# Kernel optimization log

Hardware: AMD Instinct MI355X
Metric: run time of the kernel (lower is better)

The kernel has to match this reference:

```python
import jax, jax.numpy as jnp
import numpy as np
import math

EPS = 1e-5
N_HEAD = 16

def act_quant(x):
    # BitNet per-token int8 absmax quant-dequant with straight-through estimator
    scale = 127.0 / jnp.clip(jnp.max(jnp.abs(x), axis=-1, keepdims=True), EPS)
    q = jnp.clip(jnp.round(x * scale), -128.0, 127.0) / scale
    return x + jax.lax.stop_gradient(q - x)

def bit_linear(x, W):
    # BitNet b1.58 ternary weight quant (per-tensor mean-absmax scale), STE
    s = jnp.clip(jnp.mean(jnp.abs(W)), EPS)
    Wq = jnp.clip(jnp.round(W / s), -1.0, 1.0) * s
    Wq = W + jax.lax.stop_gradient(Wq - W)
    return x @ Wq.T

def setup_inputs() -> dict:
    key = jax.random.key(0)
    ks = jax.random.split(key, 5)
    B, T, C = 2, 2048, 2048
    x = jax.random.normal(ks[0], (B, T, C), dtype=jnp.float32)
    std = 1.0 / math.sqrt(C)
    Wq = jax.random.normal(ks[1], (C, C), dtype=jnp.float32) * std
    Wk = jax.random.normal(ks[2], (C, C), dtype=jnp.float32) * std
    Wv = jax.random.normal(ks[3], (C, C), dtype=jnp.float32) * std
    Wp = jax.random.normal(ks[4], (C, C), dtype=jnp.float32) * std
    return {"x": x, "Wq": Wq, "Wk": Wk, "Wv": Wv, "Wp": Wp}

def reference(x, Wq, Wk, Wv, Wp):
    B, T, C = x.shape
    H = N_HEAD
    D = C // H
    xq = act_quant(x)
    # [B, T, C] -> [B, H, T, D]
    def heads(t):
        return t.reshape(B, T, H, D).transpose(0, 2, 1, 3)
    q = act_quant(heads(bit_linear(xq, Wq)))
    k = act_quant(heads(bit_linear(xq, Wk)))
    v = act_quant(heads(bit_linear(xq, Wv)))
    scores = jnp.einsum('bhtd,bhsd->bhts', q, k) * (1.0 / math.sqrt(D))
    w = act_quant(jax.nn.softmax(scores, axis=-1))  # dropout p=0.0 (eval)
    y = act_quant(jnp.einsum('bhts,bhsd->bhtd', w, v))
    y = y.transpose(0, 2, 1, 3).reshape(B, T, C)
    y = act_quant(bit_linear(y, Wp))
    return y
```

## Files before the change

kernel.cpp:

```cpp
#include <hip/hip_runtime.h>
#include <stdint.h>

namespace {

constexpr int B_ = 2, T_ = 2048, C_ = 2048, H_ = 16, D_ = 128;
constexpr int R_ = B_ * T_;
constexpr float EPSF = 1e-5f;
constexpr float INV_SQRT_D = 0.08838834764831845f;
constexpr float LOG2E = 1.4426950408889634f;
constexpr float LOG2_127 = 6.988684686772166f;

constexpr size_t OFF_WSUM = 0;
constexpr size_t OFF_SW   = 64;
constexpr size_t OFF_WT   = 256;
constexpr size_t OFF_XQ   = OFF_WT   + (size_t)4 * C_ * C_;
constexpr size_t OFF_SX   = OFF_XQ   + (size_t)R_ * C_;
constexpr size_t OFF_QKV  = OFF_SX   + (size_t)R_ * 4;
constexpr size_t OFF_SQKV = OFF_QKV  + (size_t)3 * R_ * C_;
constexpr size_t OFF_YQ   = OFF_SQKV + (size_t)3 * R_ * H_ * 4;
constexpr size_t OFF_SY   = OFF_YQ   + (size_t)R_ * C_;
constexpr size_t OFF_OUTP = OFF_SY   + (size_t)R_ * H_ * 4;
constexpr size_t OFF_VT   = OFF_OUTP;

typedef int   i32x4 __attribute__((ext_vector_type(4)));
typedef short s16x8 __attribute__((ext_vector_type(8)));
typedef float f32x4 __attribute__((ext_vector_type(4)));
typedef unsigned int u32x4 __attribute__((ext_vector_type(4)));

__device__ __forceinline__ i32x4 mfma_i8(i32x4 a, i32x4 b, i32x4 c) {
  return __builtin_amdgcn_mfma_i32_16x16x64_i8(a, b, c, 0, 0, 0);
}
__device__ __forceinline__ f32x4 mfma_bf16(s16x8 a, s16x8 b, f32x4 c) {
  return __builtin_amdgcn_mfma_f32_16x16x32_bf16(a, b, c, 0, 0, 0);
}

__device__ __forceinline__ void dma16(const void* g, void* l) {
  __builtin_amdgcn_global_load_lds(
      (const __attribute__((address_space(1))) void*)g,
      (__attribute__((address_space(3))) void*)l, 16, 0, 0);
}

#if __has_builtin(__builtin_amdgcn_exp2f)
__device__ __forceinline__ float fast_exp2(float x) { return __builtin_amdgcn_exp2f(x); }
#else
__device__ __forceinline__ float fast_exp2(float x) { return exp2f(x); }
#endif

__device__ __forceinline__ short f2bf(float f) {
  union { float f; uint32_t u; } v; v.f = f;
  uint32_t r = v.u + 0x7fffu + ((v.u >> 16) & 1u);
  return (short)(r >> 16);
}
__device__ __forceinline__ float bf2f(short h) {
  union { uint32_t u; float f; } v; v.u = ((uint32_t)(uint16_t)h) << 16;
  return v.f;
}

__global__ __launch_bounds__(256) void wabs_sum_kernel(
    const float* __restrict__ W0, const float* __restrict__ W1,
    const float* __restrict__ W2, const float* __restrict__ W3,
    double* __restrict__ wsum)
{
  const int w   = blockIdx.x >> 6;
  const int blk = blockIdx.x & 63;
  const float* W = (w == 0) ? W0 : (w == 1) ? W1 : (w == 2) ? W2 : W3;
  const float4* W4 = (const float4*)W;
  const int n4 = (C_ * C_) / 4;
  double s = 0.0;
  for (int i = blk * 256 + (int)threadIdx.x; i < n4; i += 64 * 256) {
    float4 v = W4[i];
    s += (double)fabsf(v.x) + (double)fabsf(v.y) +
         (double)fabsf(v.z) + (double)fabsf(v.w);
  }
  __shared__ double sm[256];
  sm[threadIdx.x] = s;
  __syncthreads();
  for (int o = 128; o > 0; o >>= 1) {
    if ((int)threadIdx.x < o) sm[threadIdx.x] += sm[threadIdx.x + o];
    __syncthreads();
  }
  if (threadIdx.x == 0) atomicAdd(&wsum[w], sm[0]);
}

__global__ __launch_bounds__(256) void wquant_kernel(
    const float* __restrict__ W0, const float* __restrict__ W1,
    const float* __restrict__ W2, const float* __restrict__ W3,
    const double* __restrict__ wsum, int8_t* __restrict__ Wt, float* __restrict__ sw)
{
  const int w = blockIdx.x >> 10;
  const float* W = (w == 0) ? W0 : (w == 1) ? W1 : (w == 2) ? W2 : W3;
  const int n = C_ * C_;
  const int n4 = n / 4;
  const float s = fmaxf((float)(wsum[w] * (1.0 / (double)n)), EPSF);
  const float4* W4 = (const float4*)W;
  uint32_t* dst4 = (uint32_t*)(Wt + (size_t)w * n);
  const int base = (blockIdx.x & 1023) * 256 + (int)threadIdx.x;
  for (int i = base; i < n4; i += 1024 * 256) {
    float4 v = W4[i];
    union { int8_t b[4]; uint32_t u; } pk;
    pk.b[0] = (int8_t)fminf(fmaxf(rintf(v.x / s), -1.f), 1.f);
    pk.b[1] = (int8_t)fminf(fmaxf(rintf(v.y / s), -1.f), 1.f);
    pk.b[2] = (int8_t)fminf(fmaxf(rintf(v.z / s), -1.f), 1.f);
    pk.b[3] = (int8_t)fminf(fmaxf(rintf(v.w / s), -1.f), 1.f);
    dst4[i] = pk.u;
  }
  if (base == 0) sw[w] = s;
}

__global__ __launch_bounds__(256) void xquant_kernel(
    const float* __restrict__ x, int8_t* __restrict__ xq, float* __restrict__ sx)
{
  const int r = blockIdx.x;
  const float4* xr = (const float4*)(x + (size_t)r * C_);
  float am = 0.f;
  for (int j = threadIdx.x; j < C_ / 4; j += 256) {
    float4 v = xr[j];
    am = fmaxf(am, fmaxf(fmaxf(fabsf(v.x), fabsf(v.y)),
                         fmaxf(fabsf(v.z), fabsf(v.w))));
  }
  __shared__ float sm[256];
  sm[threadIdx.x] = am;
  __syncthreads();
  for (int o = 128; o > 0; o >>= 1) {
    if ((int)threadIdx.x < o) sm[threadIdx.x] = fmaxf(sm[threadIdx.x], sm[threadIdx.x + o]);
    __syncthreads();
  }
  const float m = fmaxf(sm[0], EPSF);
  const float scale = 127.f / m;
  uint32_t* dst4 = (uint32_t*)(xq + (size_t)r * C_);
  for (int j = threadIdx.x; j < C_ / 4; j += 256) {
    float4 v = xr[j];
    union { int8_t b[4]; uint32_t u; } pk;
    pk.b[0] = (int8_t)fminf(fmaxf(rintf(v.x * scale), -128.f), 127.f);
    pk.b[1] = (int8_t)fminf(fmaxf(rintf(v.y * scale), -128.f), 127.f);
    pk.b[2] = (int8_t)fminf(fmaxf(rintf(v.z * scale), -128.f), 127.f);
    pk.b[3] = (int8_t)fminf(fmaxf(rintf(v.w * scale), -128.f), 127.f);
    dst4[j] = pk.u;
  }
  if (threadIdx.x == 0) sx[r] = m / 127.f;
}

__global__ __launch_bounds__(256) void proj_mfma_kernel(
    const int8_t* __restrict__ xq, const float* __restrict__ sx,
    const int8_t* __restrict__ Wt, const float* __restrict__ sw4,
    int8_t* __restrict__ qkv, float* __restrict__ sqkv)
{
  const int h    = blockIdx.x;
  const int r0   = blockIdx.y * 128;
  const int wsel = blockIdx.z;
  const int tid  = (int)threadIdx.x;
  const int wv   = tid >> 6;
  const int lane = tid & 63;
  const int quad = lane >> 4;
  const int l15  = lane & 15;
  const int rh   = wv >> 1, ch = wv & 1;
  const int8_t* Wm = Wt + (size_t)wsel * C_ * C_;

  __shared__ __align__(16) char As[2][8192];
  __shared__ __align__(16) char Bs[2][8192];
  __shared__ int rmaxs[128];
  if (tid < 128) rmaxs[tid] = 0;

  const int s0a   = wv * 128;
  const int rowA0 = (s0a + lane) >> 2;
  const int qdA0  = ((s0a + lane) & 3) ^ (rowA0 & 3);
  const int rowA1 = (s0a + 64 + lane) >> 2;
  const int qdA1  = ((s0a + 64 + lane) & 3) ^ (rowA1 & 3);

  auto stage = [&](int bf, int k0) {
    dma16(xq + (size_t)(r0 + rowA0) * C_ + k0 + qdA0 * 16, &As[bf][(s0a) * 16]);
    dma16(xq + (size_t)(r0 + rowA1) * C_ + k0 + qdA1 * 16, &As[bf][(s0a + 64) * 16]);
    dma16(Wm + (size_t)(h * 128 + rowA0) * C_ + k0 + qdA0 * 16, &Bs[bf][(s0a) * 16]);
    dma16(Wm + (size_t)(h * 128 + rowA1) * C_ + k0 + qdA1 * 16, &Bs[bf][(s0a + 64) * 16]);
  };

  i32x4 acc[4][4];
  #pragma unroll
  for (int i = 0; i < 4; ++i)
    #pragma unroll
    for (int j = 0; j < 4; ++j) acc[i][j] = i32x4{0, 0, 0, 0};

  stage(0, 0);
  for (int kc = 0; kc < 32; ++kc) {
    __syncthreads();
    if (kc + 1 < 32) stage((kc + 1) & 1, (kc + 1) * 64);
    const char* Ab = As[kc & 1];
    const char* Bb = Bs[kc & 1];
    i32x4 a[4], b[4];
    #pragma unroll
    for (int rt = 0; rt < 4; ++rt) {
      const int row = rh * 64 + rt * 16 + l15;
      a[rt] = *(const i32x4*)(Ab + (row * 4 + (quad ^ (row & 3))) * 16);
    }
    #pragma unroll
    for (int ct = 0; ct < 4; ++ct) {
      const int col = ch * 64 + ct * 16 + l15;
      b[ct] = *(const i32x4*)(Bb + (col * 4 + (quad ^ (col & 3))) * 16);
    }
    #pragma unroll
    for (int rt = 0; rt < 4; ++rt)
      #pragma unroll
      for (int ct = 0; ct < 4; ++ct)
        acc[rt][ct] = mfma_i8(a[rt], b[ct], acc[rt][ct]);
  }

  #pragma unroll
  for (int rt = 0; rt < 4; ++rt)
    #pragma unroll
    for (int r = 0; r < 4; ++r) {
      int m = 0;
      #pragma unroll
      for (int ct = 0; ct < 4; ++ct) {
        int v = acc[rt][ct][r];
        int av = v < 0 ? -v : v;
        m = m > av ? m : av;
      }
      #pragma unroll
      for (int mm = 1; mm < 16; mm <<= 1) {
        int o = __shfl_xor(m, mm, 64);
        m = m > o ? m : o;
      }
      if (l15 == 0) atomicMax(&rmaxs[rh * 64 + rt * 16 + quad * 4 + r], m);
    }
  __syncthreads();

  const float swv = sw4[wsel];
  #pragma unroll
  for (int rt = 0; rt < 4; ++rt)
    #pragma unroll
    for (int r = 0; r < 4; ++r) {
      const int rowl = rh * 64 + rt * 16 + quad * 4 + r;
      const int rglob = r0 + rowl;
      const int mN = rmaxs[rowl];
      const float qscale = (mN > 0) ? 127.f / (float)mN : 0.f;
      const int bb = rglob >> 11;
      const int tt = rglob & (T_ - 1);
      const size_t obase = ((size_t)(bb * H_ + h) * T_ + tt) * D_;
      #pragma unroll
      for (int ct = 0; ct < 4; ++ct) {
        const int col = ch * 64 + ct * 16 + l15;
        float q = rintf((float)acc[rt][ct][r] * qscale);
        q = fminf(fmaxf(q, -128.f), 127.f);
        qkv[(size_t)wsel * R_ * C_ + obase + col] = (int8_t)q;
      }
      if (ch == 0 && l15 == 0) {
        float maxq = (float)mN * sx[rglob] * swv;
        sqkv[(size_t)wsel * R_ * H_ + (size_t)(bb * H_ + h) * T_ + tt] =
            fmaxf(maxq, EPSF) / 127.f;
      }
    }
}

__global__ __launch_bounds__(256) void vtrans_kernel(
    const int8_t* __restrict__ vq, const float* __restrict__ sv,
    short* __restrict__ vT)
{
  const int bh = blockIdx.y;
  const int s0 = blockIdx.x * 64;
  const int tid = (int)threadIdx.x;
  __shared__ __align__(16) int8_t Vs[64][144];
  __shared__ float svs[64];
  const int8_t* vbase = vq + ((size_t)bh * T_ + s0) * D_;
  #pragma unroll
  for (int it = 0; it < 2; ++it) {
    int idx = tid + it * 256;
    int row = idx >> 3, seg = idx & 7;
    *(uint4*)(&Vs[row][seg * 16]) = *(const uint4*)(vbase + row * 128 + seg * 16);
  }
  if (tid < 64) svs[tid] = sv[(size_t)bh * T_ + s0 + tid];
  __syncthreads();
  const int d    = tid >> 1;
  const int half = tid & 1;
  const int kh   = half * 32;
  uint32_t oh[16], ol[16];
  #pragma unroll
  for (int i = 0; i < 32; i += 2) {
    const int k0 = kh + i, k1 = kh + i + 1;
    float v0 = (float)(int)Vs[k0][d] * svs[k0];
    float v1 = (float)(int)Vs[k1][d] * svs[k1];
    short h0 = f2bf(v0), h1 = f2bf(v1);
    short l0 = f2bf(v0 - bf2f(h0)), l1 = f2bf(v1 - bf2f(h1));
    oh[i >> 1] = (uint32_t)(uint16_t)h0 | ((uint32_t)(uint16_t)h1 << 16);
    ol[i >> 1] = (uint32_t)(uint16_t)l0 | ((uint32_t)(uint16_t)l1 << 16);
  }
  const int c = (s0 >> 5) + half;
  char* out = (char*)vT + ((((size_t)bh * 128 + d) * 64 + (size_t)c) << 7);
  const int par = d & 7;
  #pragma unroll
  for (int g = 0; g < 4; ++g) {
    uint4 hi, lo;
    hi.x = oh[2 * g];     hi.y = oh[2 * g + 1];
    hi.z = oh[2 * g + 8]; hi.w = oh[2 * g + 9];
    lo.x = ol[2 * g];     lo.y = ol[2 * g + 1];
    lo.z = ol[2 * g + 8]; lo.w = ol[2 * g + 9];
    *(uint4*)(out + (((2 * g + par) & 7) << 4))     = hi;
    *(uint4*)(out + (((2 * g + 1 + par) & 7) << 4)) = lo;
  }
}

__global__ __launch_bounds__(256, 2) void attn_mfma_kernel(
    const int8_t* __restrict__ qq, const int8_t* __restrict__ kq,
    const float* __restrict__ sq, const float* __restrict__ sk,
    const short* __restrict__ vT,
    int8_t* __restrict__ yq, float* __restrict__ sy)
{
  const int bh  = blockIdx.x;
  const int t0  = blockIdx.y * 128;
  const int tid = (int)threadIdx.x;
  const int w    = tid >> 6;
  const int lane = tid & 63;
  const int quad = lane >> 4;
  const int l15  = lane & 15;

  __shared__ __align__(16) char smem[69632];
  float* sks = (float*)(smem + 61440);

  const int qrow0 = t0 + 32 * w;

  const int8_t* kq_bh = kq + (size_t)bh * T_ * D_;
  const char*   vb    = (const char*)vT + ((size_t)bh << 20);

  const int kslot = w * 64 + lane;
  const int kkey  = kslot >> 3;
  const int ksrc  = ((kslot & 7) ^ (kkey & 7)) * 16;
  auto stageK = [&](int buf, int cc) {
    dma16(kq_bh + (size_t)(cc * 32 + kkey) * 128 + ksrc,
          smem + buf * 4096 + (w * 64) * 16);
  };

  const size_t vlane = (size_t)(w * 32 + (lane >> 3)) * 8192 + (size_t)((lane & 7) * 16);
  auto stageV = [&](int buf, int cc) {
    char* dst = smem + 12288 + buf * 16384 + (w * 32) * 128;
    const char* src = vb + vlane + (size_t)cc * 128;
    #pragma unroll
    for (int j = 0; j < 4; ++j)
      dma16(src + (size_t)(j * 8) * 8192, dst + j * 1024);
  };

  {
    const float* skg = sk + (size_t)bh * T_;
    dma16(skg + (w * 2 + 0) * 256 + lane * 4, smem + 61440 + (w * 2 + 0) * 1024);
    dma16(skg + (w * 2 + 1) * 256 + lane * 4, smem + 61440 + (w * 2 + 1) * 1024);
  }
  stageK(0, 0);
  stageV(0, 0);

  i32x4 qf[2][2];
  #pragma unroll
  for (int qt = 0; qt < 2; ++qt)
    #pragma unroll
    for (int hf = 0; hf < 2; ++hf)
      qf[qt][hf] = *(const i32x4*)(qq + ((size_t)bh * T_ + qrow0 + qt * 16 + l15) * D_ +
                                   hf * 64 + quad * 16);
  float f0[2];
  #pragma unroll
  for (int qt = 0; qt < 2; ++qt)
    f0[qt] = sq[(size_t)bh * T_ + qrow0 + qt * 16 + l15] * INV_SQRT_D;

  __syncthreads();

  const int8_t* kqb = kq_bh + (size_t)(l15 * D_ + quad * 16);

  float rx[2][4];
  #pragma unroll
  for (int qt = 0; qt < 2; ++qt)
    #pragma unroll
    for (int r = 0; r < 4; ++r) rx[qt][r] = -3e38f;

  for (int s0 = 0; s0 < T_; s0 += 64) {
    #pragma unroll
    for (int kt = 0; kt < 4; ++kt) {
      const f32x4 skv = *(const f32x4*)(sks + s0 + kt * 16 + quad * 4);
      const i32x4 ka = *(const i32x4*)(kqb + (size_t)(s0 + kt * 16) * D_);
      const i32x4 kb = *(const i32x4*)(kqb + (size_t)(s0 + kt * 16) * D_ + 64);
      #pragma unroll
      for (int qt = 0; qt < 2; ++qt) {
        i32x4 c = i32x4{0, 0, 0, 0};
        c = mfma_i8(ka, qf[qt][0], c);
        c = mfma_i8(kb, qf[qt][1], c);
        #pragma unroll
        for (int r = 0; r < 4; ++r)
          rx[qt][r] = fmaxf(rx[qt][r], (float)c[r] * skv[r]);
      }
    }
  }
  float f1[2], g[2];
  #pragma unroll
  for (int qt = 0; qt < 2; ++qt) {
    float m = fmaxf(fmaxf(rx[qt][0], rx[qt][1]), fmaxf(rx[qt][2], rx[qt][3]));
    m = fmaxf(m, __shfl_xor(m, 16, 64));
    m = fmaxf(m, __shfl_xor(m, 32, 64));
    f1[qt] = f0[qt] * LOG2E;
    g[qt]  = LOG2_127 - (m * f0[qt]) * LOG2E;
  }

  float zac[2][4] = {};
  f32x4 yacc[2][8];
  #pragma unroll
  for (int qt = 0; qt < 2; ++qt)
    #pragma unroll
    for (int dt = 0; dt < 8; ++dt) yacc[qt][dt] = f32x4{0.f, 0.f, 0.f, 0.f};

  const int seg_hi = ((2 * quad + l15) & 7) << 4;
  const int seg_lo = ((2 * quad + 1 + l15) & 7) << 4;

  int bc = 0, bn = 1;
  for (int c = 0; c < 64; ++c) {
    const int s0k = c * 32;
    if (c + 1 < 64) {
      stageK(bn, c + 1);
      stageV(bn, c + 1);
      asm volatile("s_waitcnt vmcnt(5)" ::: "memory");
    } else {
      asm volatile("s_waitcnt vmcnt(0)" ::: "memory");
    }
    __builtin_amdgcn_s_barrier();
    asm volatile("" ::: "memory");

    const char* Kb = smem + bc * 4096;
    uint32_t wdw[2][2][2];
    #pragma unroll
    for (int kt = 0; kt < 2; ++kt) {
      const f32x4 skv = *(const f32x4*)(sks + s0k + kt * 16 + quad * 4);
      const int key = kt * 16 + l15;
      const i32x4 ka = *(const i32x4*)(Kb + key * 128 + ((quad ^ (key & 7)) << 4));
      const i32x4 kb = *(const i32x4*)(Kb + key * 128 + (((quad + 4) ^ (key & 7)) << 4));
      #pragma unroll
      for (int qt = 0; qt < 2; ++qt) {
        i32x4 cc = i32x4{0, 0, 0, 0};
        cc = mfma_i8(ka, qf[qt][0], cc);
        cc = mfma_i8(kb, qf[qt][1], cc);
        float wq_[4];
        #pragma unroll
        for (int r = 0; r < 4; ++r) {
          float t = (float)cc[r] * skv[r];
          float wu = fast_exp2(fmaf(t, f1[qt], g[qt]));
          zac[qt][r] += wu;
          wq_[r] = rintf(wu);
        }
        wdw[qt][kt][0] = (__float_as_uint(wq_[0]) >> 16) |
                         (__float_as_uint(wq_[1]) & 0xffff0000u);
        wdw[qt][kt][1] = (__float_as_uint(wq_[2]) >> 16) |
                         (__float_as_uint(wq_[3]) & 0xffff0000u);
      }
    }

    s16x8 wf[2];
    #pragma unroll
    for (int qt = 0; qt < 2; ++qt) {
      u32x4 tw;
      tw[0] = wdw[qt][0][0]; tw[1] = wdw[qt][0][1];
      tw[2] = wdw[qt][1][0]; tw[3] = wdw[qt][1][1];
      wf[qt] = __builtin_bit_cast(s16x8, tw);
    }

    const char* Vc = smem + 12288 + bc * 16384;
    __builtin_amdgcn_s_setprio(1);
    #pragma unroll
    for (int dt = 0; dt < 8; ++dt) {
      const char* rowp = Vc + (dt * 16 + l15) * 128;
      const s16x8 vh = *(const s16x8*)(rowp + seg_hi);
      const s16x8 vl = *(const s16x8*)(rowp + seg_lo);
      yacc[0][dt] = mfma_bf16(wf[0], vh, yacc[0][dt]);
      yacc[0][dt] = mfma_bf16(wf[0], vl, yacc[0][dt]);
      yacc[1][dt] = mfma_bf16(wf[1], vh, yacc[1][dt]);
      yacc[1][dt] = mfma_bf16(wf[1], vl, yacc[1][dt]);
    }
    __builtin_amdgcn_s_setprio(0);

    bc = bn; bn = (bn == 2) ? 0 : bn + 1;
  }

  float zq[2];
  #pragma unroll
  for (int qt = 0; qt < 2; ++qt) {
    float z = (zac[qt][0] + zac[qt][1]) + (zac[qt][2] + zac[qt][3]);
    z += __shfl_xor(z, 16, 64);
    z += __shfl_xor(z, 32, 64);
    zq[qt] = z;
  }

  const int b = bh >> 4;
  const int h = bh & 15;
  #pragma unroll
  for (int qt = 0; qt < 2; ++qt)
    #pragma unroll
    for (int r = 0; r < 4; ++r) {
      const float zr = __shfl(zq[qt], quad * 4 + r, 64);
      float ym = 0.f;
      #pragma unroll
      for (int dt = 0; dt < 8; ++dt) ym = fmaxf(ym, fabsf(yacc[qt][dt][r]));
      #pragma unroll
      for (int mm = 1; mm < 16; mm <<= 1) ym = fmaxf(ym, __shfl_xor(ym, mm, 64));
      const float invz = 1.f / zr;
      const float ymt = fmaxf(ym * invz, EPSF);
      const float fs = 127.f / ymt;
      const int tglob = t0 + 32 * w + qt * 16 + quad * 4 + r;
      const size_t rowbase = ((size_t)(b * T_ + tglob)) * C_ + h * D_;
      #pragma unroll
      for (int dt = 0; dt < 8; ++dt) {
        float yv = yacc[qt][dt][r] * invz;
        float qv = fminf(fmaxf(rintf(yv * fs), -128.f), 127.f);
        yq[rowbase + dt * 16 + l15] = (int8_t)qv;
      }
      if (l15 == 0)
        sy[(size_t)(b * T_ + tglob) * H_ + h] = ymt / 127.f;
    }
}

__global__ __launch_bounds__(256) void outproj_mfma_kernel(
    const int8_t* __restrict__ yq, const float* __restrict__ sy,
    const int8_t* __restrict__ Wt, const float* __restrict__ sw4,
    float* __restrict__ outp)
{
  const int n0  = blockIdx.x * 64;
  const int r0  = blockIdx.y * 128;
  const int tid = (int)threadIdx.x;
  const int wv   = tid >> 6;
  const int lane = tid & 63;
  const int quad = lane >> 4;
  const int l15  = lane & 15;
  const int rh   = wv >> 1, ch = wv & 1;
  const int8_t* Wm = Wt + (size_t)3 * C_ * C_;

  __shared__ __align__(16) char As[2][8192];
  __shared__ __align__(16) char Bs[2][4096];
  __shared__ float sYs[128][16];
  for (int idx = tid; idx < 128 * 16; idx += 256)
    sYs[idx >> 4][idx & 15] = sy[(size_t)(r0 + (idx >> 4)) * H_ + (idx & 15)];

  const int s0a   = wv * 128;
  const int rowA0 = (s0a + lane) >> 2;
  const int qdA0  = ((s0a + lane) & 3) ^ (rowA0 & 3);
  const int rowA1 = (s0a + 64 + lane) >> 2;
  const int qdA1  = ((s0a + 64 + lane) & 3) ^ (rowA1 & 3);
  const int sb    = wv * 64 + lane;
  const int colB  = sb >> 2;
  const int qdB   = (sb & 3) ^ (colB & 3);

  auto stage = [&](int bf, int k0) {
    dma16(yq + (size_t)(r0 + rowA0) * C_ + k0 + qdA0 * 16, &As[bf][(s0a) * 16]);
    dma16(yq + (size_t)(r0 + rowA1) * C_ + k0 + qdA1 * 16, &As[bf][(s0a + 64) * 16]);
    dma16(Wm + (size_t)(n0 + colB) * C_ + k0 + qdB * 16, &Bs[bf][(wv * 64) * 16]);
  };

  i32x4 iacc[4][2];
  f32x4 facc[4][2];
  #pragma unroll
  for (int i = 0; i < 4; ++i)
    #pragma unroll
    for (int j = 0; j < 2; ++j) { iacc[i][j] = i32x4{0,0,0,0}; facc[i][j] = f32x4{0.f,0.f,0.f,0.f}; }

  stage(0, 0);
  for (int kc = 0; kc < 32; ++kc) {
    __syncthreads();
    if (kc + 1 < 32) stage((kc + 1) & 1, (kc + 1) * 64);
    const char* Ab = As[kc & 1];
    const char* Bb = Bs[kc & 1];
    i32x4 a[4], b[2];
    #pragma unroll
    for (int rt = 0; rt < 4; ++rt) {
      const int row = rh * 64 + rt * 16 + l15;
      a[rt] = *(const i32x4*)(Ab + (row * 4 + (quad ^ (row & 3))) * 16);
    }
    #pragma unroll
    for (int ct = 0; ct < 2; ++ct) {
      const int col = ch * 32 + ct * 16 + l15;
      b[ct] = *(const i32x4*)(Bb + (col * 4 + (quad ^ (col & 3))) * 16);
    }
    #pragma unroll
    for (int rt = 0; rt < 4; ++rt)
      #pragma unroll
      for (int ct = 0; ct < 2; ++ct)
        iacc[rt][ct] = mfma_i8(a[rt], b[ct], iacc[rt][ct]);
    if (kc & 1) {
      const int hd = kc >> 1;
      #pragma unroll
      for (int rt = 0; rt < 4; ++rt)
        #pragma unroll
        for (int r = 0; r < 4; ++r) {
          const float s = sYs[rh * 64 + rt * 16 + quad * 4 + r][hd];
          #pragma unroll
          for (int ct = 0; ct < 2; ++ct)
            facc[rt][ct][r] += (float)iacc[rt][ct][r] * s;
        }
      #pragma unroll
      for (int rt = 0; rt < 4; ++rt)
        #pragma unroll
        for (int ct = 0; ct < 2; ++ct) iacc[rt][ct] = i32x4{0,0,0,0};
    }
  }
  const float swp = sw4[3];
  #pragma unroll
  for (int rt = 0; rt < 4; ++rt)
    #pragma unroll
    for (int r = 0; r < 4; ++r) {
      const int rowl = rh * 64 + rt * 16 + quad * 4 + r;
      #pragma unroll
      for (int ct = 0; ct < 2; ++ct)
        outp[(size_t)(r0 + rowl) * C_ + n0 + ch * 32 + ct * 16 + l15] =
            facc[rt][ct][r] * swp;
    }
}

__global__ __launch_bounds__(256) void final_quant_kernel(
    const float* __restrict__ outp, float* __restrict__ out)
{
  const int r = blockIdx.x;
  const float4* xr = (const float4*)(outp + (size_t)r * C_);
  float am = 0.f;
  for (int j = threadIdx.x; j < C_ / 4; j += 256) {
    float4 v = xr[j];
    am = fmaxf(am, fmaxf(fmaxf(fabsf(v.x), fabsf(v.y)),
                         fmaxf(fabsf(v.z), fabsf(v.w))));
  }
  __shared__ float sm[256];
  sm[threadIdx.x] = am;
  __syncthreads();
  for (int o = 128; o > 0; o >>= 1) {
    if ((int)threadIdx.x < o) sm[threadIdx.x] = fmaxf(sm[threadIdx.x], sm[threadIdx.x + o]);
    __syncthreads();
  }
  const float m = fmaxf(sm[0], EPSF);
  const float scale = 127.f / m;
  const float inv = m / 127.f;
  float4* o4 = (float4*)(out + (size_t)r * C_);
  for (int j = threadIdx.x; j < C_ / 4; j += 256) {
    float4 v = xr[j];
    float4 o;
    o.x = fminf(fmaxf(rintf(v.x * scale), -128.f), 127.f) * inv;
    o.y = fminf(fmaxf(rintf(v.y * scale), -128.f), 127.f) * inv;
    o.z = fminf(fmaxf(rintf(v.z * scale), -128.f), 127.f) * inv;
    o.w = fminf(fmaxf(rintf(v.w * scale), -128.f), 127.f) * inv;
    o4[j] = o;
  }
}

}

extern "C" void kernel_launch(void* const* d_in, const int* in_sizes, int n_in,
                              void* d_out, int out_size, void* d_ws, size_t ws_size,
                              hipStream_t stream)
{
  (void)in_sizes; (void)n_in; (void)out_size; (void)ws_size;
  const float* x  = (const float*)d_in[0];
  const float* W0 = (const float*)d_in[1];
  const float* W1 = (const float*)d_in[2];
  const float* W2 = (const float*)d_in[3];
  const float* W3 = (const float*)d_in[4];

  char* ws = (char*)d_ws;
  double* wsum = (double*)(ws + OFF_WSUM);
  float*  swv  = (float*) (ws + OFF_SW);
  int8_t* Wt   = (int8_t*)(ws + OFF_WT);
  int8_t* xq   = (int8_t*)(ws + OFF_XQ);
  float*  sx   = (float*) (ws + OFF_SX);
  int8_t* qkv  = (int8_t*)(ws + OFF_QKV);
  float*  sqkv = (float*) (ws + OFF_SQKV);
  int8_t* yqp  = (int8_t*)(ws + OFF_YQ);
  float*  syp  = (float*) (ws + OFF_SY);
  float*  outp = (float*) (ws + OFF_OUTP);
  short*  vT   = (short*) (ws + OFF_VT);

  hipMemsetAsync(d_ws, 0, 256, stream);
  hipLaunchKernelGGL(wabs_sum_kernel, dim3(256), dim3(256), 0, stream, W0, W1, W2, W3, wsum);
  hipLaunchKernelGGL(wquant_kernel, dim3(4096), dim3(256), 0, stream, W0, W1, W2, W3, wsum, Wt, swv);
  hipLaunchKernelGGL(xquant_kernel, dim3(R_), dim3(256), 0, stream, x, xq, sx);
  hipLaunchKernelGGL(proj_mfma_kernel, dim3(H_, R_ / 128, 3), dim3(256), 0, stream,
                     xq, sx, Wt, swv, qkv, sqkv);
  hipLaunchKernelGGL(vtrans_kernel, dim3(T_ / 64, B_ * H_), dim3(256), 0, stream,
                     qkv + (size_t)2 * R_ * C_, sqkv + (size_t)2 * R_ * H_, vT);
  hipLaunchKernelGGL(attn_mfma_kernel, dim3(B_ * H_, T_ / 128), dim3(256), 0, stream,
                     qkv, qkv + (size_t)R_ * C_,
                     sqkv, sqkv + (size_t)R_ * H_,
                     vT, yqp, syp);
  hipLaunchKernelGGL(outproj_mfma_kernel, dim3(C_ / 64, R_ / 128), dim3(256), 0, stream,
                     yqp, syp, Wt, swv, outp);
  hipLaunchKernelGGL(final_quant_kernel, dim3(R_), dim3(256), 0, stream, outp, (float*)d_out);
}
```

Measured before the change: 446.4 us.

## Move attention row-max pass into a separate split-key kernel

The first pass of the attention kernel, which computes each query row's score maximum over all keys, moves into a new rowmax_kernel. In that kernel each block handles 64 queries, its four waves each take a quarter of the keys, and the partial maxima are combined through shared memory. The attention kernel then reads the stored row maxima and runs only the second pass. The aim is more parallelism and register reuse for the max pass, at the cost of an extra launch and a scratch buffer placed in the xq region, which is dead by then.

```diff
diff --git a/kernel.cpp b/kernel.cpp
--- a/kernel.cpp
+++ b/kernel.cpp
@@ -251,6 +251,74 @@
     }
 }
 
+__global__ __launch_bounds__(256) void rowmax_kernel(
+    const int8_t* __restrict__ qq, const int8_t* __restrict__ kq,
+    const float* __restrict__ sk, float* __restrict__ rmax)
+{
+  const int bh  = blockIdx.x;
+  const int q0  = blockIdx.y * 64;
+  const int tid = (int)threadIdx.x;
+  const int w    = tid >> 6;
+  const int lane = tid & 63;
+  const int quad = lane >> 4;
+  const int l15  = lane & 15;
+
+  i32x4 qf[4][2];
+  #pragma unroll
+  for (int qt = 0; qt < 4; ++qt)
+    #pragma unroll
+    for (int hf = 0; hf < 2; ++hf)
+      qf[qt][hf] = *(const i32x4*)(qq + ((size_t)bh * T_ + q0 + qt * 16 + l15) * D_ +
+                                   hf * 64 + quad * 16);
+
+  const int8_t* kqb = kq + (size_t)bh * T_ * D_ + (size_t)(l15 * D_ + quad * 16);
+  const float*  skb = sk + (size_t)bh * T_ + quad * 4;
+
+  float rx[4][4];
+  #pragma unroll
+  for (int qt = 0; qt < 4; ++qt)
+    #pragma unroll
+    for (int r = 0; r < 4; ++r) rx[qt][r] = -3e38f;
+
+  const int sbase = w * 512;
+  for (int st = 0; st < 8; ++st) {
+    const int s0 = sbase + st * 64;
+    #pragma unroll
+    for (int kt = 0; kt < 4; ++kt) {
+      const f32x4 skv = *(const f32x4*)(skb + s0 + kt * 16);
+      const i32x4 ka = *(const i32x4*)(kqb + (size_t)(s0 + kt * 16) * D_);
+      const i32x4 kb = *(const i32x4*)(kqb + (size_t)(s0 + kt * 16) * D_ + 64);
+      #pragma unroll
+      for (int qt = 0; qt < 4; ++qt) {
+        i32x4 c = i32x4{0, 0, 0, 0};
+        c = mfma_i8(ka, qf[qt][0], c);
+        c = mfma_i8(kb, qf[qt][1], c);
+        #pragma unroll
+        for (int r = 0; r < 4; ++r)
+          rx[qt][r] = fmaxf(rx[qt][r], (float)c[r] * skv[r]);
+      }
+    }
+  }
+
+  __shared__ float wmx[4][4][16];
+  #pragma unroll
+  for (int qt = 0; qt < 4; ++qt) {
+    float m = fmaxf(fmaxf(rx[qt][0], rx[qt][1]), fmaxf(rx[qt][2], rx[qt][3]));
+    m = fmaxf(m, __shfl_xor(m, 16, 64));
+    m = fmaxf(m, __shfl_xor(m, 32, 64));
+    if (quad == 0) wmx[w][qt][l15] = m;
+  }
+  __syncthreads();
+  if (tid < 64) {
+    #pragma unroll
+    for (int qt = 0; qt < 4; ++qt) {
+      float mm = fmaxf(fmaxf(wmx[0][qt][l15], wmx[1][qt][l15]),
+                       fmaxf(wmx[2][qt][l15], wmx[3][qt][l15]));
+      if (quad == 0) rmax[(size_t)bh * T_ + q0 + qt * 16 + l15] = mm;
+    }
+  }
+}
+
 __global__ __launch_bounds__(256) void vtrans_kernel(
     const int8_t* __restrict__ vq, const float* __restrict__ sv,
     short* __restrict__ vT)
@@ -301,7 +369,7 @@
 __global__ __launch_bounds__(256, 2) void attn_mfma_kernel(
     const int8_t* __restrict__ qq, const int8_t* __restrict__ kq,
     const float* __restrict__ sq, const float* __restrict__ sk,
-    const short* __restrict__ vT,
+    const short* __restrict__ vT, const float* __restrict__ rmax,
     int8_t* __restrict__ yq, float* __restrict__ sy)
 {
   const int bh  = blockIdx.x;
@@ -359,37 +427,10 @@
 
   __syncthreads();
 
-  const int8_t* kqb = kq_bh + (size_t)(l15 * D_ + quad * 16);
-
-  float rx[2][4];
-  #pragma unroll
-  for (int qt = 0; qt < 2; ++qt)
-    #pragma unroll
-    for (int r = 0; r < 4; ++r) rx[qt][r] = -3e38f;
-
-  for (int s0 = 0; s0 < T_; s0 += 64) {
-    #pragma unroll
-    for (int kt = 0; kt < 4; ++kt) {
-      const f32x4 skv = *(const f32x4*)(sks + s0 + kt * 16 + quad * 4);
-      const i32x4 ka = *(const i32x4*)(kqb + (size_t)(s0 + kt * 16) * D_);
-      const i32x4 kb = *(const i32x4*)(kqb + (size_t)(s0 + kt * 16) * D_ + 64);
-      #pragma unroll
-      for (int qt = 0; qt < 2; ++qt) {
-        i32x4 c = i32x4{0, 0, 0, 0};
-        c = mfma_i8(ka, qf[qt][0], c);
-        c = mfma_i8(kb, qf[qt][1], c);
-        #pragma unroll
-        for (int r = 0; r < 4; ++r)
-          rx[qt][r] = fmaxf(rx[qt][r], (float)c[r] * skv[r]);
-      }
-    }
-  }
   float f1[2], g[2];
   #pragma unroll
   for (int qt = 0; qt < 2; ++qt) {
-    float m = fmaxf(fmaxf(rx[qt][0], rx[qt][1]), fmaxf(rx[qt][2], rx[qt][3]));
-    m = fmaxf(m, __shfl_xor(m, 16, 64));
-    m = fmaxf(m, __shfl_xor(m, 32, 64));
+    const float m = rmax[(size_t)bh * T_ + qrow0 + qt * 16 + l15];
     f1[qt] = f0[qt] * LOG2E;
     g[qt]  = LOG2_127 - (m * f0[qt]) * LOG2E;
   }
@@ -661,6 +702,7 @@
   float*  syp  = (float*) (ws + OFF_SY);
   float*  outp = (float*) (ws + OFF_OUTP);
   short*  vT   = (short*) (ws + OFF_VT);
+  float*  rmx  = (float*) (ws + OFF_XQ);
 
   hipMemsetAsync(d_ws, 0, 256, stream);
   hipLaunchKernelGGL(wabs_sum_kernel, dim3(256), dim3(256), 0, stream, W0, W1, W2, W3, wsum);
@@ -668,12 +710,14 @@
   hipLaunchKernelGGL(xquant_kernel, dim3(R_), dim3(256), 0, stream, x, xq, sx);
   hipLaunchKernelGGL(proj_mfma_kernel, dim3(H_, R_ / 128, 3), dim3(256), 0, stream,
                      xq, sx, Wt, swv, qkv, sqkv);
+  hipLaunchKernelGGL(rowmax_kernel, dim3(B_ * H_, T_ / 64), dim3(256), 0, stream,
+                     qkv, qkv + (size_t)R_ * C_, sqkv + (size_t)R_ * H_, rmx);
   hipLaunchKernelGGL(vtrans_kernel, dim3(T_ / 64, B_ * H_), dim3(256), 0, stream,
                      qkv + (size_t)2 * R_ * C_, sqkv + (size_t)2 * R_ * H_, vT);
   hipLaunchKernelGGL(attn_mfma_kernel, dim3(B_ * H_, T_ / 128), dim3(256), 0, stream,
                      qkv, qkv + (size_t)R_ * C_,
                      sqkv, sqkv + (size_t)R_ * H_,
-                     vT, yqp, syp);
+                     vT, rmx, yqp, syp);
   hipLaunchKernelGGL(outproj_mfma_kernel, dim3(C_ / 64, R_ / 128), dim3(256), 0, stream,
                      yqp, syp, Wt, swv, outp);
   hipLaunchKernelGGL(final_quant_kernel, dim3(R_), dim3(256), 0, stream, outp, (float*)d_out);
```

Result: no change. 446.4 us (-0.0%).
